# Kernel optimization log

Measured on AMD Instinct MI355X. Metric: run time of the kernel, lower is better.

## Reference

```python
import jax, jax.numpy as jnp
import numpy as np

N_QUBITS = 7
N_LAYERS = 2
DIM = 2 ** N_QUBITS  # 128
NORM_FACTOR = 1.0


def _cnot_gather_idx(n):
    # CNOT chain (0,1),(1,2),...,(n-2,n-1) plus wraparound (n-1,0).
    # new_state[x] = old_state[idx[x]]; apply gates in reverse to arange.
    gates = [(i, i + 1) for i in range(n - 1)] + [(n - 1, 0)]
    idx = np.arange(2 ** n)
    for c, t in reversed(gates):
        cbit = 1 << (n - 1 - c)  # pennylane wire 0 = most significant bit
        tbit = 1 << (n - 1 - t)
        idx = np.where((idx & cbit) > 0, idx ^ tbit, idx)
    return jnp.asarray(idx)

CNOT_IDX = _cnot_gather_idx(N_QUBITS)


def silu(x):
    return x * jax.nn.sigmoid(x)


def cayley(A_real, A_imag):
    # Hermitianize then Cayley transform -> unitary, per layer. [L,D,D]
    A = A_real.astype(jnp.complex64) + 1j * A_imag.astype(jnp.complex64)
    A = A + jnp.conj(jnp.swapaxes(A, -1, -2))
    I = jnp.eye(DIM, dtype=A.dtype)
    return jnp.matmul(A - 1j * I, jnp.linalg.inv(A + 1j * I))


def _single_qubit_gate(theta_x, theta_y):
    # combined G = RY(theta_y) @ RX(theta_x) applied to every qubit
    cx, sx = jnp.cos(theta_x / 2), jnp.sin(theta_x / 2)
    cy, sy = jnp.cos(theta_y / 2), jnp.sin(theta_y / 2)
    RX = jnp.stack([jnp.stack([cx + 0j, -1j * sx]), jnp.stack([-1j * sx, cx + 0j])])
    RY = jnp.stack([jnp.stack([cy + 0j, -sy + 0j]), jnp.stack([sy + 0j, cy + 0j])])
    return RY @ RX


def quantum_evolve(psi, coeffs, q_mats):
    # psi: [N, DIM] complex64 normalized state vectors
    N = psi.shape[0]
    for j in range(N_LAYERS):
        psi = psi @ q_mats[j].T  # QubitUnitary: new = U @ old
        G = _single_qubit_gate(coeffs[j, 0], coeffs[j, 1])
        psi = psi.reshape((N,) + (2,) * N_QUBITS)
        for ax in range(1, N_QUBITS + 1):
            psi = jnp.moveaxis(jnp.tensordot(G, psi, axes=((1,), (ax,))), 0, ax)
        psi = psi.reshape(N, DIM)
        psi = psi[:, CNOT_IDX]  # CNOT chain is a fixed basis permutation
    return psi


def setup_inputs() -> dict:
    key = jax.random.key(0)
    ks = jax.random.split(key, 16)
    N, E = 50000, 800000
    in_nf, hid, out_nf = 128, 128, 128
    h = jax.random.normal(ks[0], (N, in_nf), dtype=jnp.float32)
    edge_index = jax.random.randint(ks[1], (2, E), 0, N)
    s = 0.05
    W_e1 = jax.random.normal(ks[2], (2 * in_nf, hid), dtype=jnp.float32) * s
    b_e1 = jnp.zeros((hid,), dtype=jnp.float32)
    W_e2 = jax.random.normal(ks[3], (hid, hid), dtype=jnp.float32) * s
    b_e2 = jnp.zeros((hid,), dtype=jnp.float32)
    W_enc = jax.random.normal(ks[4], (hid + in_nf, DIM), dtype=jnp.float32) * s
    b_enc = jnp.zeros((DIM,), dtype=jnp.float32)
    coeffs = jax.random.normal(ks[5], (N_LAYERS, 2), dtype=jnp.float32) * 0.1
    A_real = jax.random.normal(ks[6], (N_LAYERS, DIM, DIM), dtype=jnp.float32) * 0.01
    A_imag = jax.random.normal(ks[7], (N_LAYERS, DIM, DIM), dtype=jnp.float32) * 0.01
    W_dec = jax.random.normal(ks[8], (DIM, out_nf), dtype=jnp.float32) * s
    b_dec = jnp.zeros((out_nf,), dtype=jnp.float32)
    return {"h": h, "edge_index": edge_index, "W_e1": W_e1, "b_e1": b_e1,
            "W_e2": W_e2, "b_e2": b_e2, "W_enc": W_enc, "b_enc": b_enc,
            "coeffs": coeffs, "A_real": A_real, "A_imag": A_imag,
            "W_dec": W_dec, "b_dec": b_dec}


def reference(h, edge_index, W_e1, b_e1, W_e2, b_e2, W_enc, b_enc,
              coeffs, A_real, A_imag, W_dec, b_dec):
    row, col = edge_index[0], edge_index[1]
    # edge model: mij = MLP([h_src, h_tgt])
    e = jnp.concatenate([h[row], h[col]], axis=1)  # [E, 2*in_nf]
    e = silu(e @ W_e1 + b_e1)
    edge_feat = silu(e @ W_e2 + b_e2)  # [E, hid]
    # node model: scatter-sum aggregation over destination `row`
    agg = jax.ops.segment_sum(edge_feat, row, num_segments=h.shape[0]) / NORM_FACTOR
    q_input = jnp.concatenate([h, agg], axis=1) @ W_enc + b_enc  # [N, DIM]
    norm = jnp.sqrt(jnp.sum(q_input ** 2, axis=1, keepdims=True) + 1e-12)
    psi = (q_input / norm).astype(jnp.complex64)
    q_mats = cayley(A_real, A_imag)  # [L, DIM, DIM] unitary
    psi = quantum_evolve(psi, coeffs, q_mats)
    out = h + (jnp.real(psi) @ W_dec + b_dec)
    return out, edge_feat
```

## Files before the change

kernel.cpp:

```cpp
#include <hip/hip_runtime.h>
#include <math.h>

#define N_NODES 50000
#define N_EDGES 800000
#define NS_ITERS 2

typedef __attribute__((ext_vector_type(8))) short bf16x8;
typedef __attribute__((ext_vector_type(2))) short shortx2;
typedef __attribute__((ext_vector_type(4))) float f32x4;

__device__ __forceinline__ float silu_f(float x) {
    return x / (1.0f + __expf(-x));
}

__device__ __forceinline__ unsigned short f2bf(float x) {
    union { float f; unsigned u; } v; v.f = x;
    unsigned r = v.u + 0x7FFFu + ((v.u >> 16) & 1u);
    return (unsigned short)(r >> 16);
}

__device__ __forceinline__ void atomic_pk_add_bf16(short* addr, shortx2 v) {
    typedef shortx2 __attribute__((address_space(1)))* gp1;
    __builtin_amdgcn_global_atomic_fadd_v2bf16((gp1)(unsigned long long)addr, v);
}

__global__ __launch_bounds__(256) void hbf16_kernel(const float* __restrict__ h,
                                                    short* __restrict__ hbf) {
    int i = blockIdx.x * 256 + threadIdx.x;
    const float4* h4 = (const float4*)h;
    float4 v0 = h4[i * 2], v1 = h4[i * 2 + 1];
    bf16x8 b;
    b[0] = (short)f2bf(v0.x); b[1] = (short)f2bf(v0.y);
    b[2] = (short)f2bf(v0.z); b[3] = (short)f2bf(v0.w);
    b[4] = (short)f2bf(v1.x); b[5] = (short)f2bf(v1.y);
    b[6] = (short)f2bf(v1.z); b[7] = (short)f2bf(v1.w);
    ((bf16x8*)hbf)[i] = b;
}

__global__ __launch_bounds__(1024) void hmat_kernel(const float* __restrict__ A_real,
                                                    const float* __restrict__ A_imag,
                                                    float* __restrict__ H,
                                                    float* __restrict__ X) {
    const int L = blockIdx.x;
    const int t = threadIdx.x;
    const float* ar = A_real + L * 16384;
    const float* ai = A_imag + L * 16384;
    float* hre = H + L * 32768;
    float* him = hre + 16384;
    float* xre = X + L * 32768;
    float* xim = xre + 16384;
    for (int q = 0; q < 16; ++q) {
        int idx = t + 1024 * q;
        int i = idx >> 7, j = idx & 127;
        float hr = ar[idx] + ar[j * 128 + i];
        float hi = ai[idx] - ai[j * 128 + i];
        hre[idx] = hr;
        him[idx] = hi;
        xre[idx] = hr;
        xim[idx] = hi - (i == j ? 1.0f : 0.0f);
    }
}

__global__ __launch_bounds__(512) void ns_t_kernel(const float* __restrict__ H,
                                                   const float* __restrict__ X,
                                                   float* __restrict__ T) {
    const int L = blockIdx.x >> 5;
    const int t = threadIdx.x;
    const int i = (blockIdx.x & 31) * 4 + (t >> 7);
    const int j = t & 127;
    const float* hre = H + L * 32768;
    const float* him = hre + 16384;
    const float* xre = X + L * 32768;
    const float* xim = xre + 16384;
    float accr = 0.f, acci = 0.f;
    #pragma unroll 4
    for (int k = 0; k < 128; ++k) {
        float hr = hre[i * 128 + k], hi = him[i * 128 + k];
        float xr = xre[k * 128 + j], xi = xim[k * 128 + j];
        accr += hr * xr - hi * xi;
        acci += hr * xi + hi * xr;
    }
    T[L * 32768 + i * 128 + j]         = accr - xim[i * 128 + j];
    T[L * 32768 + 16384 + i * 128 + j] = acci + xre[i * 128 + j];
}

__global__ __launch_bounds__(512) void ns_x_kernel(const float* __restrict__ X,
                                                   const float* __restrict__ T,
                                                   float* __restrict__ Xout) {
    const int L = blockIdx.x >> 5;
    const int t = threadIdx.x;
    const int i = (blockIdx.x & 31) * 4 + (t >> 7);
    const int j = t & 127;
    const float* xre = X + L * 32768;
    const float* xim = xre + 16384;
    const float* tre = T + L * 32768;
    const float* tim = tre + 16384;
    float accr = 0.f, acci = 0.f;
    #pragma unroll 4
    for (int k = 0; k < 128; ++k) {
        float xr = xre[i * 128 + k], xi = xim[i * 128 + k];
        float tr = tre[k * 128 + j], ti = tim[k * 128 + j];
        accr += xr * tr - xi * ti;
        acci += xr * ti + xi * tr;
    }
    Xout[L * 32768 + i * 128 + j]         = 2.0f * xre[i * 128 + j] - accr;
    Xout[L * 32768 + 16384 + i * 128 + j] = 2.0f * xim[i * 128 + j] - acci;
}

__global__ __launch_bounds__(1024) void gateperm_kernel(const float* __restrict__ X,
                                                        const float* __restrict__ coeffs,
                                                        float* __restrict__ Y) {
    __shared__ float Mre[128 * 129];
    __shared__ float Mim[128 * 129];
    const int L = blockIdx.x;
    const int t = threadIdx.x;
    const float* xre = X + L * 32768;
    const float* xim = xre + 16384;

    for (int q = 0; q < 16; ++q) {
        int idx = t + 1024 * q;
        int i = idx >> 7, j = idx & 127;
        Mre[i * 129 + j] = (i == j ? 1.0f : 0.0f) + 2.0f * xim[idx];
        Mim[i * 129 + j] = -2.0f * xre[idx];
    }
    __syncthreads();

    const float tx = coeffs[2 * L + 0] * 0.5f;
    const float ty = coeffs[2 * L + 1] * 0.5f;
    const float cx = cosf(tx), sx = sinf(tx), cy = cosf(ty), sy = sinf(ty);
    const float G00r = cx * cy, G00i = sx * sy;
    const float G01r = -cx * sy, G01i = -sx * cy;
    const float G10r = cx * sy, G10i = -sx * cy;
    const float G11r = cx * cy, G11i = -sx * sy;

    for (int st = 0; st < 7; ++st) {
        int b = 1 << st;
        #pragma unroll
        for (int p = 0; p < 8; ++p) {
            int pid = t + 1024 * p;
            int col = pid & 127, ph = pid >> 7;
            int i0 = ((ph >> st) << (st + 1)) | (ph & (b - 1));
            int i1 = i0 | b;
            float v0r = Mre[i0 * 129 + col], v0i = Mim[i0 * 129 + col];
            float v1r = Mre[i1 * 129 + col], v1i = Mim[i1 * 129 + col];
            Mre[i0 * 129 + col] = G00r * v0r - G00i * v0i + G01r * v1r - G01i * v1i;
            Mim[i0 * 129 + col] = G00r * v0i + G00i * v0r + G01r * v1i + G01i * v1r;
            Mre[i1 * 129 + col] = G10r * v0r - G10i * v0i + G11r * v1r - G11i * v1i;
            Mim[i1 * 129 + col] = G10r * v0i + G10i * v0r + G11r * v1i + G11i * v1r;
        }
        __syncthreads();
    }

    const int cs[7] = {6, 5, 4, 3, 2, 1, 0};
    const int ts[7] = {0, 6, 5, 4, 3, 2, 1};
    float* yre = Y + L * 32768;
    float* yim = yre + 16384;
    for (int q = 0; q < 16; ++q) {
        int idx = t + 1024 * q;
        int ii_ = idx >> 7, col = idx & 127;
        int s = ii_;
        #pragma unroll
        for (int m = 0; m < 7; ++m) {
            int cbit = 1 << (6 - cs[m]);
            int tbit = 1 << (6 - ts[m]);
            if (s & cbit) s ^= tbit;
        }
        yre[idx] = Mre[s * 129 + col];
        yim[idx] = Mim[s * 129 + col];
    }
}

__global__ __launch_bounds__(512) void combine1_kernel(const float* __restrict__ Y,
                                                       float* __restrict__ ReM) {
    __shared__ float q1r[16384];
    __shared__ float q1i[16384];
    const int t = threadIdx.x;
    const float* q1re = Y;
    const float* q1im = Y + 16384;
    const float* q2re = Y + 32768;
    const float* q2im = Y + 49152;
    for (int q = 0; q < 32; ++q) {
        q1r[t + 512 * q] = q1re[t + 512 * q];
        q1i[t + 512 * q] = q1im[t + 512 * q];
    }
    __syncthreads();
    int i = blockIdx.x * 4 + (t >> 7);
    int j = t & 127;
    float acc = 0.f;
    for (int k = 0; k < 128; ++k) {
        acc += q2re[i * 128 + k] * q1r[k * 128 + j] - q2im[i * 128 + k] * q1i[k * 128 + j];
    }
    ReM[i * 128 + j] = acc;
}

__global__ __launch_bounds__(512) void combine2_kernel(const float* __restrict__ ReM,
                                                       const float* __restrict__ W_dec,
                                                       short* __restrict__ Dt) {
    __shared__ float ml[16384];
    __shared__ float wl[16384];
    const int t = threadIdx.x;
    for (int q = 0; q < 32; ++q) {
        ml[t + 512 * q] = ReM[t + 512 * q];
        wl[t + 512 * q] = W_dec[t + 512 * q];
    }
    __syncthreads();
    int k = blockIdx.x * 4 + (t >> 7);
    int j = t & 127;
    float acc = 0.f;
    for (int i = 0; i < 128; ++i) {
        acc += ml[i * 128 + k] * wl[i * 128 + j];
    }
    Dt[j * 128 + k] = (short)f2bf(acc);
}

__global__ __launch_bounds__(1024, 4) void edge_kernel(const short* __restrict__ hbf,
                                                       const int* __restrict__ ei,
                                                       const float* __restrict__ W_e1,
                                                       const float* __restrict__ b_e1,
                                                       const float* __restrict__ W_e2,
                                                       const float* __restrict__ b_e2,
                                                       float* __restrict__ ef_out,
                                                       short* __restrict__ agg_bf) {
    __shared__ short w1t[128 * 256];
    __shared__ short w2t[128 * 128];
    __shared__ short c1s[16][1024];

    const int t = threadIdx.x;
    const int lane = t & 63;
    const int w = t >> 6;
    const int l15 = lane & 15;
    const int kg = lane >> 4;

    {
        const float4* w1_4 = (const float4*)W_e1;
        for (int q = 0; q < 8; ++q) {
            int idx4 = t + 1024 * q;
            int k = idx4 >> 5, j4 = idx4 & 31;
            float4 v = w1_4[idx4];
            int j = j4 * 4;
            w1t[(j + 0) * 256 + (k ^ (((j + 0) & 7) << 3))] = (short)f2bf(v.x);
            w1t[(j + 1) * 256 + (k ^ (((j + 1) & 7) << 3))] = (short)f2bf(v.y);
            w1t[(j + 2) * 256 + (k ^ (((j + 2) & 7) << 3))] = (short)f2bf(v.z);
            w1t[(j + 3) * 256 + (k ^ (((j + 3) & 7) << 3))] = (short)f2bf(v.w);
        }
        const float4* w2_4 = (const float4*)W_e2;
        for (int q = 0; q < 4; ++q) {
            int idx4 = t + 1024 * q;
            int k = idx4 >> 5, j4 = idx4 & 31;
            float4 v = w2_4[idx4];
            int j = j4 * 4;
            w2t[(j + 0) * 128 + (k ^ (((j + 0) & 7) << 3))] = (short)f2bf(v.x);
            w2t[(j + 1) * 128 + (k ^ (((j + 1) & 7) << 3))] = (short)f2bf(v.y);
            w2t[(j + 2) * 128 + (k ^ (((j + 2) & 7) << 3))] = (short)f2bf(v.z);
            w2t[(j + 3) * 128 + (k ^ (((j + 3) & 7) << 3))] = (short)f2bf(v.w);
        }
    }
    float b1v[8], b2v[8];
    #pragma unroll
    for (int nf = 0; nf < 8; ++nf) {
        b1v[nf] = b_e1[nf * 16 + l15];
        b2v[nf] = b_e2[nf * 16 + l15];
    }
    __syncthreads();

    const bf16x8* hb8 = (const bf16x8*)hbf;
    short* myc1 = &c1s[w][0];
    const int NW = gridDim.x * 16;
    const int nt = N_EDGES / 16;

    int tile = blockIdx.x * 16 + w;
    if (tile >= nt) return;
    int ri = ei[tile * 16 + l15];
    int ci = ei[N_EDGES + tile * 16 + l15];
    bf16x8 a1[8];
    #pragma unroll
    for (int s = 0; s < 4; ++s) a1[s] = hb8[(size_t)ri * 16 + s * 4 + kg];
    #pragma unroll
    for (int s = 0; s < 4; ++s) a1[4 + s] = hb8[(size_t)ci * 16 + s * 4 + kg];
    int tn = tile + NW;
    bool more = (tn < nt);
    int rin = 0, cin = 0;
    if (more) {
        rin = ei[tn * 16 + l15];
        cin = ei[N_EDGES + tn * 16 + l15];
    }

    for (;;) {
        const int e0 = tile * 16;
        bf16x8 a1n[8];
        if (more) {
            #pragma unroll
            for (int s = 0; s < 4; ++s) a1n[s] = hb8[(size_t)rin * 16 + s * 4 + kg];
        }

        f32x4 acc[8];
        #pragma unroll
        for (int nf = 0; nf < 8; ++nf) acc[nf] = (f32x4){0.f, 0.f, 0.f, 0.f};
        #pragma unroll
        for (int s = 0; s < 8; ++s) {
            const int k0 = s * 32 + kg * 8;
            #pragma unroll
            for (int nf = 0; nf < 8; ++nf) {
                int brow = nf * 16 + l15;
                bf16x8 b = *(const bf16x8*)&w1t[brow * 256 + (k0 ^ ((brow & 7) << 3))];
                acc[nf] = __builtin_amdgcn_mfma_f32_16x16x32_bf16(a1[s], b, acc[nf], 0, 0, 0);
            }
        }

        if (more) {
            #pragma unroll
            for (int s = 0; s < 4; ++s) a1n[4 + s] = hb8[(size_t)cin * 16 + s * 4 + kg];
        }

        f32x4 acc2[8];
        #pragma unroll
        for (int nf = 0; nf < 8; ++nf) acc2[nf] = (f32x4){0.f, 0.f, 0.f, 0.f};
        #pragma unroll
        for (int half = 0; half < 2; ++half) {
            #pragma unroll
            for (int nfh = 0; nfh < 4; ++nfh) {
                int nf = half * 4 + nfh;
                #pragma unroll
                for (int r = 0; r < 4; ++r) {
                    int row = kg * 4 + r;
                    int c = nfh * 16 + l15;
                    myc1[row * 64 + (c ^ ((row & 7) << 3))] =
                        (short)f2bf(silu_f(acc[nf][r] + b1v[nf]));
                }
            }
            #pragma unroll
            for (int s2l = 0; s2l < 2; ++s2l) {
                int k0h = s2l * 32 + kg * 8;
                bf16x8 a2 = *(const bf16x8*)&myc1[l15 * 64 + (k0h ^ ((l15 & 7) << 3))];
                int k0g = half * 64 + k0h;
                #pragma unroll
                for (int nf = 0; nf < 8; ++nf) {
                    int brow = nf * 16 + l15;
                    bf16x8 b = *(const bf16x8*)&w2t[brow * 128 + (k0g ^ ((brow & 7) << 3))];
                    acc2[nf] = __builtin_amdgcn_mfma_f32_16x16x32_bf16(a2, b, acc2[nf], 0, 0, 0);
                }
            }
        }

        int rw[4];
        #pragma unroll
        for (int r = 0; r < 4; ++r) rw[r] = __shfl(ri, kg * 4 + r);
        #pragma unroll
        for (int r = 0; r < 4; ++r) {
            int erow = kg * 4 + r;
            float* efp = ef_out + (size_t)(e0 + erow) * 128;
            short* agp = agg_bf + (size_t)rw[r] * 128;
            #pragma unroll
            for (int nf = 0; nf < 8; ++nf) {
                int col = nf * 16 + l15;
                float v = silu_f(acc2[nf][r] + b2v[nf]);
                __builtin_nontemporal_store(v, efp + col);
                float vn = __shfl_xor(v, 1);
                if ((l15 & 1) == 0) {
                    shortx2 pk;
                    pk.x = (short)f2bf(v);
                    pk.y = (short)f2bf(vn);
                    atomic_pk_add_bf16(agp + col, pk);
                }
            }
        }

        if (!more) break;
        tile = tn;
        ri = rin;
        #pragma unroll
        for (int s = 0; s < 8; ++s) a1[s] = a1n[s];
        tn = tile + NW;
        more = (tn < nt);
        if (more) {
            rin = ei[tn * 16 + l15];
            cin = ei[N_EDGES + tn * 16 + l15];
        }
    }
}

__global__ __launch_bounds__(512, 2) void node_kernel(const short* __restrict__ hbf,
                                                      const short* __restrict__ agg_bf,
                                                      const float* __restrict__ W_enc,
                                                      const float* __restrict__ b_enc,
                                                      const short* __restrict__ Dt_bf,
                                                      const float* __restrict__ b_dec,
                                                      const float* __restrict__ h,
                                                      float* __restrict__ out) {
    __shared__ short wet[128 * 256];
    __shared__ short dtl[128 * 128];
    __shared__ short c1s[8][2048];

    const int t = threadIdx.x;
    const int lane = t & 63;
    const int w = t >> 6;
    const int l15 = lane & 15;
    const int kg = lane >> 4;

    {
        const float4* we4 = (const float4*)W_enc;
        for (int q = 0; q < 16; ++q) {
            int idx4 = t + 512 * q;
            int k = idx4 >> 5, j4 = idx4 & 31;
            float4 v = we4[idx4];
            int j = j4 * 4;
            wet[(j + 0) * 256 + (k ^ (((j + 0) & 7) << 3))] = (short)f2bf(v.x);
            wet[(j + 1) * 256 + (k ^ (((j + 1) & 7) << 3))] = (short)f2bf(v.y);
            wet[(j + 2) * 256 + (k ^ (((j + 2) & 7) << 3))] = (short)f2bf(v.z);
            wet[(j + 3) * 256 + (k ^ (((j + 3) & 7) << 3))] = (short)f2bf(v.w);
        }
        const int4* s4 = (const int4*)Dt_bf;
        for (int q = 0; q < 4; ++q) {
            int idx4 = t + 512 * q;
            int j = idx4 >> 4, c = idx4 & 15;
            int k0 = c * 8;
            int4 v = s4[idx4];
            *(int4*)&dtl[j * 128 + (k0 ^ ((j & 7) << 3))] = v;
        }
    }
    float bj1[8], bj2[8];
    #pragma unroll
    for (int nf = 0; nf < 8; ++nf) {
        bj1[nf] = b_enc[nf * 16 + l15];
        bj2[nf] = b_dec[nf * 16 + l15];
    }
    __syncthreads();

    const bf16x8* hb8 = (const bf16x8*)hbf;
    const bf16x8* ab8 = (const bf16x8*)agg_bf;
    short* myc1 = &c1s[w][0];
    const int NW = gridDim.x * 8;
    const int nt = N_NODES / 16;

    for (int tile = blockIdx.x * 8 + w; tile < nt; tile += NW) {
        const int node = tile * 16 + l15;
        bf16x8 a[8];
        #pragma unroll
        for (int s = 0; s < 4; ++s) a[s] = hb8[(size_t)node * 16 + s * 4 + kg];
        #pragma unroll
        for (int s = 0; s < 4; ++s) a[4 + s] = ab8[(size_t)node * 16 + s * 4 + kg];

        f32x4 acc[8];
        #pragma unroll
        for (int nf = 0; nf < 8; ++nf) acc[nf] = (f32x4){0.f, 0.f, 0.f, 0.f};
        #pragma unroll
        for (int s = 0; s < 8; ++s) {
            const int k0 = s * 32 + kg * 8;
            #pragma unroll
            for (int nf = 0; nf < 8; ++nf) {
                int brow = nf * 16 + l15;
                bf16x8 b = *(const bf16x8*)&wet[brow * 256 + (k0 ^ ((brow & 7) << 3))];
                acc[nf] = __builtin_amdgcn_mfma_f32_16x16x32_bf16(a[s], b, acc[nf], 0, 0, 0);
            }
        }

        float nr[4] = {0.f, 0.f, 0.f, 0.f};
        #pragma unroll
        for (int nf = 0; nf < 8; ++nf) {
            #pragma unroll
            for (int r = 0; r < 4; ++r) {
                acc[nf][r] += bj1[nf];
                nr[r] += acc[nf][r] * acc[nf][r];
            }
        }
        #pragma unroll
        for (int r = 0; r < 4; ++r) {
            nr[r] += __shfl_xor(nr[r], 1);
            nr[r] += __shfl_xor(nr[r], 2);
            nr[r] += __shfl_xor(nr[r], 4);
            nr[r] += __shfl_xor(nr[r], 8);
            nr[r] = 1.0f / sqrtf(nr[r] + 1e-12f);
        }

        #pragma unroll
        for (int nf = 0; nf < 8; ++nf) {
            #pragma unroll
            for (int r = 0; r < 4; ++r) {
                int row = kg * 4 + r;
                int col = nf * 16 + l15;
                myc1[row * 128 + (col ^ ((row & 7) << 3))] = (short)f2bf(acc[nf][r] * nr[r]);
            }
        }

        f32x4 acc2[8];
        #pragma unroll
        for (int nf = 0; nf < 8; ++nf) acc2[nf] = (f32x4){0.f, 0.f, 0.f, 0.f};
        #pragma unroll
        for (int s = 0; s < 4; ++s) {
            const int k0 = s * 32 + kg * 8;
            bf16x8 a2 = *(const bf16x8*)&myc1[l15 * 128 + (k0 ^ ((l15 & 7) << 3))];
            #pragma unroll
            for (int nf = 0; nf < 8; ++nf) {
                int brow = nf * 16 + l15;
                bf16x8 b = *(const bf16x8*)&dtl[brow * 128 + (k0 ^ ((brow & 7) << 3))];
                acc2[nf] = __builtin_amdgcn_mfma_f32_16x16x32_bf16(a2, b, acc2[nf], 0, 0, 0);
            }
        }

        #pragma unroll
        for (int r = 0; r < 4; ++r) {
            size_t rowb = (size_t)(tile * 16 + kg * 4 + r) * 128;
            #pragma unroll
            for (int nf = 0; nf < 8; ++nf) {
                int col = nf * 16 + l15;
                out[rowb + col] = h[rowb + col] + acc2[nf][r] + bj2[nf];
            }
        }
    }
}

extern "C" void kernel_launch(void* const* d_in, const int* in_sizes, int n_in,
                              void* d_out, int out_size, void* d_ws, size_t ws_size,
                              hipStream_t stream) {
    const float* h      = (const float*)d_in[0];
    const int*   ei     = (const int*)d_in[1];
    const float* W_e1   = (const float*)d_in[2];
    const float* b_e1   = (const float*)d_in[3];
    const float* W_e2   = (const float*)d_in[4];
    const float* b_e2   = (const float*)d_in[5];
    const float* W_enc  = (const float*)d_in[6];
    const float* b_enc  = (const float*)d_in[7];
    const float* coeffs = (const float*)d_in[8];
    const float* A_real = (const float*)d_in[9];
    const float* A_imag = (const float*)d_in[10];
    const float* W_dec  = (const float*)d_in[11];
    const float* b_dec  = (const float*)d_in[12];

    float* out    = (float*)d_out;
    float* ef_out = out + (size_t)N_NODES * 128;

    short* agg_bf = (short*)d_ws;
    short* h_bf   = agg_bf + (size_t)N_NODES * 128;
    float* small  = (float*)(h_bf + (size_t)N_NODES * 128);
    float* Ybuf   = small;
    float* ReM    = Ybuf + 65536;
    float* Hbuf   = ReM + 16384;
    float* Xa     = Hbuf + 65536;
    float* Xb     = Xa + 65536;
    float* Tbuf   = Xb + 65536;
    short* Dt_bf  = (short*)(Tbuf + 65536);

    hipMemsetAsync(agg_bf, 0, (size_t)N_NODES * 128 * sizeof(short), stream);

    hbf16_kernel<<<3125, 256, 0, stream>>>(h, h_bf);

    hmat_kernel<<<2, 1024, 0, stream>>>(A_real, A_imag, Hbuf, Xa);
    float* xc = Xa;
    float* xn = Xb;
    for (int it = 0; it < NS_ITERS; ++it) {
        ns_t_kernel<<<64, 512, 0, stream>>>(Hbuf, xc, Tbuf);
        ns_x_kernel<<<64, 512, 0, stream>>>(xc, Tbuf, xn);
        float* tmp = xc; xc = xn; xn = tmp;
    }
    gateperm_kernel<<<2, 1024, 0, stream>>>(xc, coeffs, Ybuf);
    combine1_kernel<<<32, 512, 0, stream>>>(Ybuf, ReM);
    combine2_kernel<<<32, 512, 0, stream>>>(ReM, W_dec, Dt_bf);

    edge_kernel<<<256, 1024, 0, stream>>>(h_bf, ei, W_e1, b_e1, W_e2, b_e2, ef_out, agg_bf);

    node_kernel<<<196, 512, 0, stream>>>(h_bf, agg_bf, W_enc, b_enc, Dt_bf, b_dec, h, out);
}
```

Measured before the change: 604.5 us.

## Replace bf16 atomic scatter with CSR-based gather aggregation kernel

Removes the packed bf16 global atomics from the edge kernel and instead builds a CSR grouping of edges by destination node (count, single-block scan, fill). A separate per-node kernel then gathers and sums the fp32 edge features and writes bf16 aggregates without atomics. The edge kernel loop is also simplified: it drops the register double-buffering of the next tile's node features and loads them at the top of each iteration. This trades atomic contention and bf16 accumulation error for extra launches, a serial scan, and rereading 400MB of edge features from memory.

```diff
diff --git a/kernel.cpp b/kernel.cpp
--- a/kernel.cpp
+++ b/kernel.cpp
@@ -6,7 +6,6 @@
 #define NS_ITERS 2
 
 typedef __attribute__((ext_vector_type(8))) short bf16x8;
-typedef __attribute__((ext_vector_type(2))) short shortx2;
 typedef __attribute__((ext_vector_type(4))) float f32x4;
 
 __device__ __forceinline__ float silu_f(float x) {
@@ -17,11 +16,6 @@
     union { float f; unsigned u; } v; v.f = x;
     unsigned r = v.u + 0x7FFFu + ((v.u >> 16) & 1u);
     return (unsigned short)(r >> 16);
-}
-
-__device__ __forceinline__ void atomic_pk_add_bf16(short* addr, shortx2 v) {
-    typedef shortx2 __attribute__((address_space(1)))* gp1;
-    __builtin_amdgcn_global_atomic_fadd_v2bf16((gp1)(unsigned long long)addr, v);
 }
 
 __global__ __launch_bounds__(256) void hbf16_kernel(const float* __restrict__ h,
@@ -35,6 +29,87 @@
     b[4] = (short)f2bf(v1.x); b[5] = (short)f2bf(v1.y);
     b[6] = (short)f2bf(v1.z); b[7] = (short)f2bf(v1.w);
     ((bf16x8*)hbf)[i] = b;
+}
+
+__global__ __launch_bounds__(256) void count_kernel(const int* __restrict__ ei,
+                                                    int* __restrict__ cnt) {
+    int e = blockIdx.x * 256 + threadIdx.x;
+    if (e < N_EDGES) atomicAdd(&cnt[ei[e]], 1);
+}
+
+__global__ __launch_bounds__(1024) void scan_kernel(const int* __restrict__ cnt,
+                                                    int* __restrict__ base,
+                                                    int* __restrict__ cursor) {
+    __shared__ int sA[1024];
+    __shared__ int sB[1024];
+    const int t = threadIdx.x;
+    const int CH = 49;
+    int s = 0;
+    #pragma unroll 4
+    for (int i = 0; i < CH; ++i) {
+        int idx = t * CH + i;
+        if (idx < N_NODES) s += cnt[idx];
+    }
+    sA[t] = s;
+    __syncthreads();
+    int* src = sA;
+    int* dst = sB;
+    for (int off = 1; off < 1024; off <<= 1) {
+        int v = src[t];
+        if (t >= off) v += src[t - off];
+        dst[t] = v;
+        __syncthreads();
+        int* tmp = src; src = dst; dst = tmp;
+    }
+    int run = (t == 0) ? 0 : src[t - 1];
+    for (int i = 0; i < CH; ++i) {
+        int idx = t * CH + i;
+        if (idx < N_NODES) {
+            base[idx] = run;
+            cursor[idx] = run;
+            run += cnt[idx];
+        }
+    }
+}
+
+__global__ __launch_bounds__(256) void fill_kernel(const int* __restrict__ ei,
+                                                   int* __restrict__ cursor,
+                                                   int* __restrict__ elist) {
+    int e = blockIdx.x * 256 + threadIdx.x;
+    if (e < N_EDGES) {
+        int slot = atomicAdd(&cursor[ei[e]], 1);
+        elist[slot] = e;
+    }
+}
+
+__global__ __launch_bounds__(256) void agg_kernel(const float* __restrict__ ef,
+                                                  const int* __restrict__ base,
+                                                  const int* __restrict__ cnt,
+                                                  const int* __restrict__ elist,
+                                                  short* __restrict__ agg_bf) {
+    int wv = blockIdx.x * 4 + (threadIdx.x >> 6);
+    if (wv >= N_NODES) return;
+    const int lane = threadIdx.x & 63;
+    const int b = base[wv];
+    const int d = cnt[wv];
+    float ax = 0.f, ay = 0.f;
+    int k = 0;
+    for (; k + 1 < d; k += 2) {
+        int e0 = elist[b + k];
+        int e1 = elist[b + k + 1];
+        float2 v0 = ((const float2*)(ef + (size_t)e0 * 128))[lane];
+        float2 v1 = ((const float2*)(ef + (size_t)e1 * 128))[lane];
+        ax += v0.x + v1.x;
+        ay += v0.y + v1.y;
+    }
+    if (k < d) {
+        int e0 = elist[b + k];
+        float2 v0 = ((const float2*)(ef + (size_t)e0 * 128))[lane];
+        ax += v0.x;
+        ay += v0.y;
+    }
+    unsigned pk = ((unsigned)f2bf(ay) << 16) | (unsigned)f2bf(ax);
+    *(unsigned*)(agg_bf + (size_t)wv * 128 + lane * 2) = pk;
 }
 
 __global__ __launch_bounds__(1024) void hmat_kernel(const float* __restrict__ A_real,
@@ -219,8 +294,7 @@
                                                        const float* __restrict__ b_e1,
                                                        const float* __restrict__ W_e2,
                                                        const float* __restrict__ b_e2,
-                                                       float* __restrict__ ef_out,
-                                                       short* __restrict__ agg_bf) {
+                                                       float* __restrict__ ef_out) {
     __shared__ short w1t[128 * 256];
     __shared__ short w2t[128 * 128];
     __shared__ short c1s[16][1024];
@@ -269,28 +343,25 @@
     const int nt = N_EDGES / 16;
 
     int tile = blockIdx.x * 16 + w;
-    if (tile >= nt) return;
-    int ri = ei[tile * 16 + l15];
-    int ci = ei[N_EDGES + tile * 16 + l15];
-    bf16x8 a1[8];
-    #pragma unroll
-    for (int s = 0; s < 4; ++s) a1[s] = hb8[(size_t)ri * 16 + s * 4 + kg];
-    #pragma unroll
-    for (int s = 0; s < 4; ++s) a1[4 + s] = hb8[(size_t)ci * 16 + s * 4 + kg];
-    int tn = tile + NW;
-    bool more = (tn < nt);
-    int rin = 0, cin = 0;
-    if (more) {
-        rin = ei[tn * 16 + l15];
-        cin = ei[N_EDGES + tn * 16 + l15];
-    }
-
-    for (;;) {
+    int ri = 0, ci = 0;
+    if (tile < nt) {
+        ri = ei[tile * 16 + l15];
+        ci = ei[N_EDGES + tile * 16 + l15];
+    }
+
+    for (; tile < nt; ) {
         const int e0 = tile * 16;
-        bf16x8 a1n[8];
-        if (more) {
-            #pragma unroll
-            for (int s = 0; s < 4; ++s) a1n[s] = hb8[(size_t)rin * 16 + s * 4 + kg];
+        bf16x8 a1[8];
+        #pragma unroll
+        for (int s = 0; s < 4; ++s) a1[s] = hb8[(size_t)ri * 16 + s * 4 + kg];
+        #pragma unroll
+        for (int s = 0; s < 4; ++s) a1[4 + s] = hb8[(size_t)ci * 16 + s * 4 + kg];
+
+        const int tn = tile + NW;
+        int ri2 = 0, ci2 = 0;
+        if (tn < nt) {
+            ri2 = ei[tn * 16 + l15];
+            ci2 = ei[N_EDGES + tn * 16 + l15];
         }
 
         f32x4 acc[8];
@@ -305,11 +376,6 @@
                 bf16x8 b = *(const bf16x8*)&w1t[brow * 256 + (k0 ^ ((brow & 7) << 3))];
                 acc[nf] = __builtin_amdgcn_mfma_f32_16x16x32_bf16(a1[s], b, acc[nf], 0, 0, 0);
             }
-        }
-
-        if (more) {
-            #pragma unroll
-            for (int s = 0; s < 4; ++s) a1n[4 + s] = hb8[(size_t)cin * 16 + s * 4 + kg];
         }
 
         f32x4 acc2[8];
@@ -342,40 +408,19 @@
             }
         }
 
-        int rw[4];
-        #pragma unroll
-        for (int r = 0; r < 4; ++r) rw[r] = __shfl(ri, kg * 4 + r);
         #pragma unroll
         for (int r = 0; r < 4; ++r) {
             int erow = kg * 4 + r;
             float* efp = ef_out + (size_t)(e0 + erow) * 128;
-            short* agp = agg_bf + (size_t)rw[r] * 128;
             #pragma unroll
             for (int nf = 0; nf < 8; ++nf) {
                 int col = nf * 16 + l15;
                 float v = silu_f(acc2[nf][r] + b2v[nf]);
                 __builtin_nontemporal_store(v, efp + col);
-                float vn = __shfl_xor(v, 1);
-                if ((l15 & 1) == 0) {
-                    shortx2 pk;
-                    pk.x = (short)f2bf(v);
-                    pk.y = (short)f2bf(vn);
-                    atomic_pk_add_bf16(agp + col, pk);
-                }
-            }
-        }
-
-        if (!more) break;
-        tile = tn;
-        ri = rin;
-        #pragma unroll
-        for (int s = 0; s < 8; ++s) a1[s] = a1n[s];
-        tn = tile + NW;
-        more = (tn < nt);
-        if (more) {
-            rin = ei[tn * 16 + l15];
-            cin = ei[N_EDGES + tn * 16 + l15];
-        }
+            }
+        }
+
+        tile = tn; ri = ri2; ci = ci2;
     }
 }
 
@@ -531,7 +576,11 @@
 
     short* agg_bf = (short*)d_ws;
     short* h_bf   = agg_bf + (size_t)N_NODES * 128;
-    float* small  = (float*)(h_bf + (size_t)N_NODES * 128);
+    int*   cnt    = (int*)(h_bf + (size_t)N_NODES * 128);
+    int*   base   = cnt + 50176;
+    int*   cursor = base + 50176;
+    int*   elist  = cursor + 50176;
+    float* small  = (float*)(elist + N_EDGES);
     float* Ybuf   = small;
     float* ReM    = Ybuf + 65536;
     float* Hbuf   = ReM + 16384;
@@ -540,9 +589,12 @@
     float* Tbuf   = Xb + 65536;
     short* Dt_bf  = (short*)(Tbuf + 65536);
 
-    hipMemsetAsync(agg_bf, 0, (size_t)N_NODES * 128 * sizeof(short), stream);
-
     hbf16_kernel<<<3125, 256, 0, stream>>>(h, h_bf);
+
+    hipMemsetAsync(cnt, 0, 50176 * sizeof(int), stream);
+    count_kernel<<<3125, 256, 0, stream>>>(ei, cnt);
+    scan_kernel<<<1, 1024, 0, stream>>>(cnt, base, cursor);
+    fill_kernel<<<3125, 256, 0, stream>>>(ei, cursor, elist);
 
     hmat_kernel<<<2, 1024, 0, stream>>>(A_real, A_imag, Hbuf, Xa);
     float* xc = Xa;
@@ -556,7 +608,9 @@
     combine1_kernel<<<32, 512, 0, stream>>>(Ybuf, ReM);
     combine2_kernel<<<32, 512, 0, stream>>>(ReM, W_dec, Dt_bf);
 
-    edge_kernel<<<256, 1024, 0, stream>>>(h_bf, ei, W_e1, b_e1, W_e2, b_e2, ef_out, agg_bf);
+    edge_kernel<<<256, 1024, 0, stream>>>(h_bf, ei, W_e1, b_e1, W_e2, b_e2, ef_out);
+
+    agg_kernel<<<12500, 256, 0, stream>>>(ef_out, base, cnt, elist, agg_bf);
 
     node_kernel<<<196, 512, 0, stream>>>(h_bf, agg_bf, W_enc, b_enc, Dt_bf, b_dec, h, out);
 }
```

Result: slower. 1.789 ms (+195.9%).
